# Optimization experiments

Hardware: AMD Instinct MI355X
Metric: run time of the kernel (lower is better)

Reference implementation:

```python
import jax, jax.numpy as jnp
import numpy as np

B, L, C, H = 16, 1024, 512, 8
D = C // H
SCALE = D ** -0.5


def setup_inputs() -> dict:
    key = jax.random.key(0)
    ks = jax.random.split(key, 16)
    s = 0.02  # weight init scale
    inp = {
        "query": jax.random.normal(ks[0], (B, L, C), jnp.float32),
        "query_pos": jax.random.normal(ks[1], (B, L, C), jnp.float32),
        "Wqc": jax.random.normal(ks[2], (C, C), jnp.float32) * s,
        "bqc": jax.random.normal(ks[3], (C,), jnp.float32) * s,
        "Wqp": jax.random.normal(ks[4], (C, C), jnp.float32) * s,
        "bqp": jax.random.normal(ks[5], (C,), jnp.float32) * s,
        "Wkc": jax.random.normal(ks[6], (C, C), jnp.float32) * s,
        "bkc": jax.random.normal(ks[7], (C,), jnp.float32) * s,
        "Wkp": jax.random.normal(ks[8], (C, C), jnp.float32) * s,
        "bkp": jax.random.normal(ks[9], (C,), jnp.float32) * s,
        "Wv": jax.random.normal(ks[10], (C, C), jnp.float32) * s,
        "bv": jax.random.normal(ks[11], (C,), jnp.float32) * s,
        "Wo": jax.random.normal(ks[12], (C, C), jnp.float32) * s,
        "bo": jax.random.normal(ks[13], (C,), jnp.float32) * s,
    }
    return inp


def reference(query, query_pos, Wqc, bqc, Wqp, bqp, Wkc, bkc, Wkp, bkp, Wv, bv, Wo, bo):
    # key = query, value = key, identity = query, key_pos = query_pos (shapes match)
    qc = query @ Wqc.T + bqc          # [B, L, C]
    qp = query_pos @ Wqp.T + bqp
    kc = query @ Wkc.T + bkc
    kp = query_pos @ Wkp.T + bkp
    v = query @ Wv.T + bv

    def split_heads(x):  # [B, L, C] -> [B, H, L, D]
        return x.reshape(B, L, H, D).transpose(0, 2, 1, 3)

    q = split_heads(qc + qp) * SCALE
    k = split_heads(kc + kp)
    vh = split_heads(v)

    attn = jnp.einsum("bhqd,bhkd->bhqk", q, k)
    attn = jax.nn.softmax(attn, axis=-1)
    out = jnp.einsum("bhqk,bhkd->bhqd", attn, vh)  # [B, H, L, D]
    out = out.transpose(0, 2, 1, 3).reshape(B, L, C)
    out = out @ Wo.T + bo
    return query + out
```

## Files before the change

### kernel.cpp

```cpp
#include <hip/hip_runtime.h>

typedef __attribute__((ext_vector_type(8))) short short8;
typedef __attribute__((ext_vector_type(4))) short short4v;
typedef __attribute__((ext_vector_type(4))) float f32x4;
typedef unsigned short u16;

#define QSCALE 0.18033688011112042f

#define BB 16
#define LL 1024
#define CC 512
#define HH 8
#define DD 64
#define MROWS (BB*LL)
#define KPROJ 1024
#define NPROJ 1536

#define WS_XCAT   0ull
#define WS_WCAT   (WS_XCAT + (size_t)MROWS*KPROJ*2)
#define WS_WO     (WS_WCAT + (size_t)NPROJ*KPROJ*2)
#define WS_BIAS   (WS_WO   + (size_t)CC*CC*2)
#define WS_QH     (WS_BIAS + 8192)
#define WS_KH     (WS_QH + (size_t)MROWS*CC*2)
#define WS_VH     (WS_KH + (size_t)MROWS*CC*2)
#define WS_OH     (WS_VH + (size_t)MROWS*CC*2)
#define WS_END    (WS_OH + (size_t)MROWS*CC*2)
#define WS_VT     WS_XCAT

__device__ inline short f2bf(float f) {
  unsigned u = __builtin_bit_cast(unsigned, f);
  u = (u + 0x7FFFu + ((u >> 16) & 1u)) >> 16;
  return (short)u;
}

__device__ inline short8 pack8(const float* src) {
  float4 a = ((const float4*)src)[0];
  float4 b = ((const float4*)src)[1];
  short8 v;
  v[0]=f2bf(a.x); v[1]=f2bf(a.y); v[2]=f2bf(a.z); v[3]=f2bf(a.w);
  v[4]=f2bf(b.x); v[5]=f2bf(b.y); v[6]=f2bf(b.z); v[7]=f2bf(b.w);
  return v;
}

__device__ inline void gload_lds16(const u16* g, char* lds_byte) {
  __builtin_amdgcn_global_load_lds(
      (const __attribute__((address_space(1))) unsigned int*)g,
      (__attribute__((address_space(3))) unsigned int*)lds_byte,
      16, 0, 0);
}


__global__ __launch_bounds__(256) void pack_x_kernel(
    const float* __restrict__ q, const float* __restrict__ qp, u16* __restrict__ xcat) {
  int o = blockIdx.x * 256 + threadIdx.x;
  int row = o >> 7;
  int kk  = (o & 127) << 3;
  const float* src = (kk < 512) ? (q + (size_t)row * 512 + kk)
                                : (qp + (size_t)row * 512 + (kk - 512));
  short8 v = pack8(src);
  *(short8*)(xcat + (size_t)row * KPROJ + kk) = v;
}

__global__ __launch_bounds__(256) void pack_w_kernel(
    const float* __restrict__ Wqc, const float* __restrict__ Wqp,
    const float* __restrict__ Wkc, const float* __restrict__ Wkp,
    const float* __restrict__ Wv,  const float* __restrict__ Wo,
    const float* __restrict__ bqc, const float* __restrict__ bqp,
    const float* __restrict__ bkc, const float* __restrict__ bkp,
    const float* __restrict__ bv,
    u16* __restrict__ wcat, u16* __restrict__ wo_bf, float* __restrict__ bias_cat) {
  int o = blockIdx.x * 256 + threadIdx.x;
  if (o < 196608) {
    int j = o >> 7;
    int kk = (o & 127) << 3;
    const float* src = nullptr;
    if (j < 512)        src = (kk < 512) ? Wqc + (size_t)j * 512 + kk : Wqp + (size_t)j * 512 + (kk - 512);
    else if (j < 1024) { int jj = j - 512;  src = (kk < 512) ? Wkc + (size_t)jj * 512 + kk : Wkp + (size_t)jj * 512 + (kk - 512); }
    else               { int jj = j - 1024; src = (kk < 512) ? Wv  + (size_t)jj * 512 + kk : nullptr; }
    short8 v = {0,0,0,0,0,0,0,0};
    if (src) v = pack8(src);
    *(short8*)(wcat + (size_t)j * KPROJ + kk) = v;
  } else if (o < 229376) {
    int o2 = o - 196608;
    int j = o2 >> 6;
    int kk = (o2 & 63) << 3;
    short8 v = pack8(Wo + (size_t)j * 512 + kk);
    *(short8*)(wo_bf + (size_t)j * 512 + kk) = v;
  }
  if (o < 1536) {
    float v;
    if (o < 512)       v = bqc[o] + bqp[o];
    else if (o < 1024) v = bkc[o - 512] + bkp[o - 512];
    else               v = bv[o - 1024];
    bias_cat[o] = v;
  }
}

template <int KDIM>
__device__ inline void gemm128_loop(const u16* __restrict__ A, const u16* __restrict__ Bw,
                                    int m0, int n0, u16* lds, f32x4 (&acc)[4][4]) {
  const int tid = threadIdx.x;
  const int lane = tid & 63, wave = tid >> 6;
  const int wr = wave >> 1, wc = wave & 1;
  const int lr = lane & 15, lg = lane >> 4;

  auto stage = [&](int buf, int t) {
    int k0 = t * 64;
    #pragma unroll
    for (int i = 0; i < 4; ++i) {
      int s = i * 256 + tid;
      int row = s >> 3, col = s & 7;
      int colp = col ^ (row & 7);
      gload_lds16(A + (size_t)(m0 + row) * KDIM + k0 + colp * 8,
                  (char*)lds + (size_t)buf * 32768 + (size_t)(i * 256 + wave * 64) * 16);
      gload_lds16(Bw + (size_t)(n0 + row) * KDIM + k0 + colp * 8,
                  (char*)lds + (size_t)buf * 32768 + 16384 + (size_t)(i * 256 + wave * 64) * 16);
    }
  };

  auto rdA = [&](int buf, int mf, int ks) {
    int rowl = wr * 64 + mf * 16 + lr;
    int ch = (ks * 4 + lg) ^ (rowl & 7);
    return *(const short8*)(lds + (size_t)buf * 16384 + (size_t)rowl * 64 + ch * 8);
  };
  auto rdB = [&](int buf, int nf, int ks) {
    int rowl = wc * 64 + nf * 16 + lr;
    int ch = (ks * 4 + lg) ^ (rowl & 7);
    return *(const short8*)(lds + (size_t)buf * 16384 + 8192 + (size_t)rowl * 64 + ch * 8);
  };

  stage(0, 0);
  asm volatile("s_waitcnt vmcnt(0)" ::: "memory");
  __builtin_amdgcn_s_barrier();

  constexpr int NT = KDIM / 64;
  int cur = 0;
  for (int t = 0; t < NT; ++t) {
    if (t + 1 < NT) stage(cur ^ 1, t + 1);
    short8 bf[4][2], af[4][2];
    #pragma unroll
    for (int nf = 0; nf < 4; ++nf)
      #pragma unroll
      for (int ks = 0; ks < 2; ++ks) bf[nf][ks] = rdB(cur, nf, ks);
    #pragma unroll
    for (int mf = 0; mf < 4; ++mf)
      #pragma unroll
      for (int ks = 0; ks < 2; ++ks) af[mf][ks] = rdA(cur, mf, ks);
    __builtin_amdgcn_s_setprio(1);
    #pragma unroll
    for (int mf = 0; mf < 4; ++mf)
      #pragma unroll
      for (int nf = 0; nf < 4; ++nf)
        #pragma unroll
        for (int ks = 0; ks < 2; ++ks)
          acc[mf][nf] = __builtin_amdgcn_mfma_f32_16x16x32_bf16(
              bf[nf][ks], af[mf][ks], acc[mf][nf], 0, 0, 0);
    __builtin_amdgcn_s_setprio(0);
    asm volatile("s_waitcnt vmcnt(0)" ::: "memory");
    __builtin_amdgcn_s_barrier();
    cur ^= 1;
  }
}

__global__ __launch_bounds__(256, 2) void proj_gemm_kernel(
    const u16* __restrict__ Xcat, const u16* __restrict__ Wcat,
    const float* __restrict__ bias_cat,
    u16* __restrict__ Qh, u16* __restrict__ Kh, u16* __restrict__ Vh) {
  __shared__ __align__(16) u16 lds[2 * 16384];

  int id0 = blockIdx.x;
  int swz = (id0 & 7) * 192 + (id0 >> 3);
  int bx = swz / 12, by = swz % 12;
  const int m0 = bx * 128, n0 = by * 128;

  const int lane = threadIdx.x & 63, wave = threadIdx.x >> 6;
  const int wr = wave >> 1, wc = wave & 1;
  const int lr = lane & 15, lg = lane >> 4;

  f32x4 acc[4][4];
  f32x4 z4 = {0.f, 0.f, 0.f, 0.f};
  #pragma unroll
  for (int mf = 0; mf < 4; ++mf)
    #pragma unroll
    for (int nf = 0; nf < 4; ++nf) acc[mf][nf] = z4;

  gemm128_loop<KPROJ>(Xcat, Wcat, m0, n0, lds, acc);

  const int cbase = n0 + wc * 64 + lg * 4;
  #pragma unroll
  for (int mf = 0; mf < 4; ++mf) {
    int lglob = m0 + wr * 64 + mf * 16 + lr;
    int bidx = lglob >> 10, lrow = lglob & 1023;
    #pragma unroll
    for (int nf = 0; nf < 4; ++nf) {
      int c = cbase + nf * 16;
      float4 bb = *(const float4*)&bias_cat[c];
      int sec = c >> 9, cj = c & 511;
      int h = cj >> 6, d0 = cj & 63;
      size_t idx = ((size_t)(bidx * HH + h) * LL + lrow) * DD + d0;
      float v0 = acc[mf][nf][0] + bb.x;
      float v1 = acc[mf][nf][1] + bb.y;
      float v2 = acc[mf][nf][2] + bb.z;
      float v3 = acc[mf][nf][3] + bb.w;
      if (sec == 0) { v0 *= QSCALE; v1 *= QSCALE; v2 *= QSCALE; v3 *= QSCALE; }
      short4v o;
      o[0] = f2bf(v0); o[1] = f2bf(v1); o[2] = f2bf(v2); o[3] = f2bf(v3);
      u16* dst = (sec == 0) ? Qh : (sec == 1) ? Kh : Vh;
      *(short4v*)&dst[idx] = o;
    }
  }
}

__global__ __launch_bounds__(256, 2) void out_gemm_kernel(
    const u16* __restrict__ Oh, const u16* __restrict__ Wo_bf,
    const float* __restrict__ bo, const float* __restrict__ query,
    float* __restrict__ out) {
  __shared__ __align__(16) u16 lds[2 * 16384];

  int id0 = blockIdx.x;
  int swz = (id0 & 7) * 64 + (id0 >> 3);
  int bx = swz / 4, by = swz % 4;
  const int m0 = bx * 128, n0 = by * 128;

  const int lane = threadIdx.x & 63, wave = threadIdx.x >> 6;
  const int wr = wave >> 1, wc = wave & 1;
  const int lr = lane & 15, lg = lane >> 4;

  f32x4 acc[4][4];
  f32x4 z4 = {0.f, 0.f, 0.f, 0.f};
  #pragma unroll
  for (int mf = 0; mf < 4; ++mf)
    #pragma unroll
    for (int nf = 0; nf < 4; ++nf) acc[mf][nf] = z4;

  gemm128_loop<CC>(Oh, Wo_bf, m0, n0, lds, acc);

  const int cbase = n0 + wc * 64 + lg * 4;
  #pragma unroll
  for (int mf = 0; mf < 4; ++mf) {
    int rw = m0 + wr * 64 + mf * 16 + lr;
    #pragma unroll
    for (int nf = 0; nf < 4; ++nf) {
      int c = cbase + nf * 16;
      float4 bb = *(const float4*)&bo[c];
      size_t idx = (size_t)rw * CC + c;
      float4 qq = *(const float4*)&query[idx];
      float4 o;
      o.x = acc[mf][nf][0] + bb.x + qq.x;
      o.y = acc[mf][nf][1] + bb.y + qq.y;
      o.z = acc[mf][nf][2] + bb.z + qq.z;
      o.w = acc[mf][nf][3] + bb.w + qq.w;
      *(float4*)&out[idx] = o;
    }
  }
}

__global__ __launch_bounds__(256) void vtrans_kernel(
    const u16* __restrict__ Vh, u16* __restrict__ Vt) {
  __shared__ u16 T[64][72];
  int bh = blockIdx.y;
  int l0 = blockIdx.x * 64;
  int t = threadIdx.x;
  const u16* src = Vh + (size_t)bh * LL * DD;
  {
    int l = t >> 2, dq = (t & 3) * 16;
    short8 v0 = *(const short8*)(src + (size_t)(l0 + l) * DD + dq);
    short8 v1 = *(const short8*)(src + (size_t)(l0 + l) * DD + dq + 8);
    #pragma unroll
    for (int j = 0; j < 8; ++j) T[dq + j][l] = (u16)v0[j];
    #pragma unroll
    for (int j = 0; j < 8; ++j) T[dq + 8 + j][l] = (u16)v1[j];
  }
  __syncthreads();
  {
    int d = t >> 2, lq = (t & 3) * 16;
    u16* dst = Vt + (size_t)bh * DD * LL + (size_t)d * LL + l0 + lq;
    *(short8*)dst = *(const short8*)&T[d][lq];
    *(short8*)(dst + 8) = *(const short8*)&T[d][lq + 8];
  }
}

__global__ __launch_bounds__(256, 2) void attn_kernel(
    const u16* __restrict__ Qh, const u16* __restrict__ Kh,
    const u16* __restrict__ Vt, u16* __restrict__ Oh) {
  __shared__ __align__(16) u16 Kl[2][64 * 64];
  __shared__ __align__(16) u16 Vl[2][64 * 64];
  __shared__ __align__(16) char Pp[4][8192];

  const int tid = threadIdx.x;
  const int lane = tid & 63, wave = tid >> 6;
  const int lr = lane & 15, lg = lane >> 4;
  const int sw = (lr & 7) * 2;
  int n = blockIdx.x;
  int rest = n >> 3;
  const int bh = (n & 7) * 16 + (rest >> 2);
  const int q0 = (rest & 3) * 256;

  const u16* Qb = Qh + (size_t)bh * LL * DD;
  const u16* Kb = Kh + (size_t)bh * LL * DD;
  const u16* Vb = Vt + (size_t)bh * DD * LL;

  short8 aq[4][2];
  #pragma unroll
  for (int m = 0; m < 4; ++m)
    #pragma unroll
    for (int s = 0; s < 2; ++s)
      aq[m][s] = *(const short8*)(Qb + (size_t)(q0 + wave * 64 + m * 16 + lr) * DD + s * 32 + lg * 8);

  f32x4 z4 = {0.f, 0.f, 0.f, 0.f};
  f32x4 oaccT[4][4];
  #pragma unroll
  for (int m = 0; m < 4; ++m)
    #pragma unroll
    for (int db = 0; db < 4; ++db) oaccT[m][db] = z4;
  float lsums[4] = {0.f, 0.f, 0.f, 0.f};

  auto stage = [&](int buf, int kt) {
    int kk0 = kt * 64;
    #pragma unroll
    for (int i = 0; i < 2; ++i) {
      int c = i * 256 + wave * 64 + lane;
      int row = c >> 3, koct = c & 7;
      int ks = koct ^ (row & 7);
      gload_lds16(Kb + (size_t)(kk0 + row) * DD + ks * 8,
                  (char*)&Kl[buf][0] + (size_t)(i * 4 + wave) * 1024);
      gload_lds16(Vb + (size_t)row * LL + kk0 + ks * 8,
                  (char*)&Vl[buf][0] + (size_t)(i * 4 + wave) * 1024);
    }
  };

  stage(0, 0);
  int cur = 0;
  char* Pw = &Pp[wave][0];
  for (int kt = 0; kt < 16; ++kt) {
    if (kt + 1 < 16) {
      stage(cur ^ 1, kt + 1);
      asm volatile("s_waitcnt vmcnt(4)" ::: "memory");
    } else {
      asm volatile("s_waitcnt vmcnt(0)" ::: "memory");
    }
    __builtin_amdgcn_s_barrier();
    __builtin_amdgcn_sched_barrier(0);

    short8 ka[2][4];
    #pragma unroll
    for (int s = 0; s < 2; ++s)
      #pragma unroll
      for (int kb = 0; kb < 4; ++kb) {
        int key = kb * 16 + lr;
        int dct = s * 4 + lg;
        ka[s][kb] = *(const short8*)((const char*)&Kl[cur][0] + (size_t)key * 128 + ((dct ^ (key & 7)) << 4));
      }
    f32x4 ps[4][4];
    #pragma unroll
    for (int m = 0; m < 4; ++m)
      #pragma unroll
      for (int kb = 0; kb < 4; ++kb) ps[m][kb] = z4;
    __builtin_amdgcn_s_setprio(1);
    #pragma unroll
    for (int s = 0; s < 2; ++s)
      #pragma unroll
      for (int kb = 0; kb < 4; ++kb)
        #pragma unroll
        for (int m = 0; m < 4; ++m)
          ps[m][kb] = __builtin_amdgcn_mfma_f32_16x16x32_bf16(ka[s][kb], aq[m][s], ps[m][kb], 0, 0, 0);
    __builtin_amdgcn_s_setprio(0);

    #pragma unroll
    for (int m = 0; m < 4; ++m) {
      #pragma unroll
      for (int kb = 0; kb < 4; ++kb) {
        float p0, p1, p2, p3;
        asm("v_exp_f32 %0, %1" : "=v"(p0) : "v"(ps[m][kb][0]));
        asm("v_exp_f32 %0, %1" : "=v"(p1) : "v"(ps[m][kb][1]));
        asm("v_exp_f32 %0, %1" : "=v"(p2) : "v"(ps[m][kb][2]));
        asm("v_exp_f32 %0, %1" : "=v"(p3) : "v"(ps[m][kb][3]));
        lsums[m] += (p0 + p1) + (p2 + p3);
        unsigned lo, hi;
        asm("v_cvt_pk_bf16_f32 %0, %1, %2" : "=v"(lo) : "v"(p0), "v"(p1));
        asm("v_cvt_pk_bf16_f32 %0, %1, %2" : "=v"(hi) : "v"(p2), "v"(p3));
        uint2 w; w.x = lo; w.y = hi;
        *(uint2*)(Pw + m * 2048 + lr * 128 + ((((kb * 4 + lg) ^ sw)) << 3)) = w;
      }
    }

    short8 bv[2][4];
    #pragma unroll
    for (int s = 0; s < 2; ++s)
      #pragma unroll
      for (int db = 0; db < 4; ++db) {
        int d = db * 16 + lr;
        int kct = s * 4 + lg;
        bv[s][db] = *(const short8*)((const char*)&Vl[cur][0] + (size_t)d * 128 + ((kct ^ (d & 7)) << 4));
      }

    asm volatile("s_waitcnt lgkmcnt(0)" ::: "memory");
    __builtin_amdgcn_sched_barrier(0);

    __builtin_amdgcn_s_setprio(1);
    #pragma unroll
    for (int m = 0; m < 4; ++m) {
      #pragma unroll
      for (int s = 0; s < 2; ++s) {
        int val0 = s * 8 + lg * 2;
        uint4 pw = *(const uint4*)(Pw + m * 2048 + lr * 128 + (((val0 ^ sw)) << 3));
        short8 ap = __builtin_bit_cast(short8, pw);
        #pragma unroll
        for (int db = 0; db < 4; ++db)
          oaccT[m][db] = __builtin_amdgcn_mfma_f32_16x16x32_bf16(bv[s][db], ap, oaccT[m][db], 0, 0, 0);
      }
    }
    __builtin_amdgcn_s_setprio(0);

    __builtin_amdgcn_s_barrier();
    cur ^= 1;
  }

  int b = bh >> 3, h = bh & 7;
  #pragma unroll
  for (int m = 0; m < 4; ++m) {
    float v = lsums[m];
    v += __shfl_xor(v, 16);
    v += __shfl_xor(v, 32);
    float inv = 1.0f / v;
    int q = q0 + wave * 64 + m * 16 + lr;
    #pragma unroll
    for (int db = 0; db < 4; ++db) {
      int d0 = db * 16 + lg * 4;
      short4v o;
      #pragma unroll
      for (int r = 0; r < 4; ++r) o[r] = f2bf(oaccT[m][db][r] * inv);
      *(short4v*)&Oh[(size_t)(b * LL + q) * CC + h * 64 + d0] = o;
    }
  }
}

extern "C" void kernel_launch(void* const* d_in, const int* in_sizes, int n_in,
                              void* d_out, int out_size, void* d_ws, size_t ws_size,
                              hipStream_t stream) {
  (void)in_sizes; (void)n_in; (void)out_size;
  const float* query = (const float*)d_in[0];
  const float* qpos  = (const float*)d_in[1];
  const float* Wqc = (const float*)d_in[2];
  const float* bqc = (const float*)d_in[3];
  const float* Wqp = (const float*)d_in[4];
  const float* bqp = (const float*)d_in[5];
  const float* Wkc = (const float*)d_in[6];
  const float* bkc = (const float*)d_in[7];
  const float* Wkp = (const float*)d_in[8];
  const float* bkp = (const float*)d_in[9];
  const float* Wv  = (const float*)d_in[10];
  const float* bv  = (const float*)d_in[11];
  const float* Wo  = (const float*)d_in[12];
  const float* bo  = (const float*)d_in[13];

  char* ws = (char*)d_ws;
  if (ws_size < WS_END) return;

  u16*   Xcat     = (u16*)(ws + WS_XCAT);
  u16*   Wcat     = (u16*)(ws + WS_WCAT);
  u16*   Wo_bf    = (u16*)(ws + WS_WO);
  float* bias_cat = (float*)(ws + WS_BIAS);
  u16*   Qh       = (u16*)(ws + WS_QH);
  u16*   Kh       = (u16*)(ws + WS_KH);
  u16*   Vh       = (u16*)(ws + WS_VH);
  u16*   Oh       = (u16*)(ws + WS_OH);
  u16*   Vtr      = (u16*)(ws + WS_VT);
  float* out      = (float*)d_out;

  pack_x_kernel<<<dim3(8192), dim3(256), 0, stream>>>(query, qpos, Xcat);
  pack_w_kernel<<<dim3(896), dim3(256), 0, stream>>>(Wqc, Wqp, Wkc, Wkp, Wv, Wo,
                                                     bqc, bqp, bkc, bkp, bv,
                                                     Wcat, Wo_bf, bias_cat);
  proj_gemm_kernel<<<dim3((MROWS / 128) * (NPROJ / 128)), dim3(256), 0, stream>>>(
      Xcat, Wcat, bias_cat, Qh, Kh, Vh);
  vtrans_kernel<<<dim3(LL / 64, BB * HH), dim3(256), 0, stream>>>(Vh, Vtr);
  attn_kernel<<<dim3(512), dim3(256), 0, stream>>>(Qh, Kh, Vtr, Oh);
  out_gemm_kernel<<<dim3((MROWS / 128) * (CC / 128)), dim3(256), 0, stream>>>(
      Oh, Wo_bf, bo, query, out);
}
```

Measured before the change: 159.4 us.

## Fuse V transpose into projection GEMM epilogue and merge pack kernels

The projection GEMM epilogue for V-column tiles now transposes the tile through LDS and writes V directly in the [b,h,d,l] layout the attention kernel consumes. This removes the separate vtrans kernel and the round trip of V through global memory. The two packing kernels are merged into one launch to save a kernel launch. The cost is extra LDS traffic and a barrier in the epilogue of the V blocks, which creates divergent work between block types.

```diff
diff --git a/kernel.cpp b/kernel.cpp
--- a/kernel.cpp
+++ b/kernel.cpp
@@ -22,10 +22,9 @@
 #define WS_BIAS   (WS_WO   + (size_t)CC*CC*2)
 #define WS_QH     (WS_BIAS + 8192)
 #define WS_KH     (WS_QH + (size_t)MROWS*CC*2)
-#define WS_VH     (WS_KH + (size_t)MROWS*CC*2)
-#define WS_OH     (WS_VH + (size_t)MROWS*CC*2)
+#define WS_VT     (WS_KH + (size_t)MROWS*CC*2)
+#define WS_OH     (WS_VT + (size_t)MROWS*CC*2)
 #define WS_END    (WS_OH + (size_t)MROWS*CC*2)
-#define WS_VT     WS_XCAT
 
 __device__ inline short f2bf(float f) {
   unsigned u = __builtin_bit_cast(unsigned, f);
@@ -49,27 +48,27 @@
       16, 0, 0);
 }
 
-
-__global__ __launch_bounds__(256) void pack_x_kernel(
-    const float* __restrict__ q, const float* __restrict__ qp, u16* __restrict__ xcat) {
-  int o = blockIdx.x * 256 + threadIdx.x;
-  int row = o >> 7;
-  int kk  = (o & 127) << 3;
-  const float* src = (kk < 512) ? (q + (size_t)row * 512 + kk)
-                                : (qp + (size_t)row * 512 + (kk - 512));
-  short8 v = pack8(src);
-  *(short8*)(xcat + (size_t)row * KPROJ + kk) = v;
-}
-
-__global__ __launch_bounds__(256) void pack_w_kernel(
+__global__ __launch_bounds__(256) void pack_all_kernel(
+    const float* __restrict__ q, const float* __restrict__ qp,
     const float* __restrict__ Wqc, const float* __restrict__ Wqp,
     const float* __restrict__ Wkc, const float* __restrict__ Wkp,
     const float* __restrict__ Wv,  const float* __restrict__ Wo,
     const float* __restrict__ bqc, const float* __restrict__ bqp,
     const float* __restrict__ bkc, const float* __restrict__ bkp,
     const float* __restrict__ bv,
-    u16* __restrict__ wcat, u16* __restrict__ wo_bf, float* __restrict__ bias_cat) {
-  int o = blockIdx.x * 256 + threadIdx.x;
+    u16* __restrict__ xcat, u16* __restrict__ wcat, u16* __restrict__ wo_bf,
+    float* __restrict__ bias_cat) {
+  if (blockIdx.x < 8192) {
+    int o = blockIdx.x * 256 + threadIdx.x;
+    int row = o >> 7;
+    int kk  = (o & 127) << 3;
+    const float* src = (kk < 512) ? (q + (size_t)row * 512 + kk)
+                                  : (qp + (size_t)row * 512 + (kk - 512));
+    short8 v = pack8(src);
+    *(short8*)(xcat + (size_t)row * KPROJ + kk) = v;
+    return;
+  }
+  int o = (blockIdx.x - 8192) * 256 + threadIdx.x;
   if (o < 196608) {
     int j = o >> 7;
     int kk = (o & 127) << 3;
@@ -165,7 +164,7 @@
 __global__ __launch_bounds__(256, 2) void proj_gemm_kernel(
     const u16* __restrict__ Xcat, const u16* __restrict__ Wcat,
     const float* __restrict__ bias_cat,
-    u16* __restrict__ Qh, u16* __restrict__ Kh, u16* __restrict__ Vh) {
+    u16* __restrict__ Qh, u16* __restrict__ Kh, u16* __restrict__ Vt) {
   __shared__ __align__(16) u16 lds[2 * 16384];
 
   int id0 = blockIdx.x;
@@ -173,7 +172,8 @@
   int bx = swz / 12, by = swz % 12;
   const int m0 = bx * 128, n0 = by * 128;
 
-  const int lane = threadIdx.x & 63, wave = threadIdx.x >> 6;
+  const int tid = threadIdx.x;
+  const int lane = tid & 63, wave = tid >> 6;
   const int wr = wave >> 1, wc = wave & 1;
   const int lr = lane & 15, lg = lane >> 4;
 
@@ -186,27 +186,57 @@
 
   gemm128_loop<KPROJ>(Xcat, Wcat, m0, n0, lds, acc);
 
-  const int cbase = n0 + wc * 64 + lg * 4;
-  #pragma unroll
-  for (int mf = 0; mf < 4; ++mf) {
-    int lglob = m0 + wr * 64 + mf * 16 + lr;
-    int bidx = lglob >> 10, lrow = lglob & 1023;
-    #pragma unroll
-    for (int nf = 0; nf < 4; ++nf) {
-      int c = cbase + nf * 16;
-      float4 bb = *(const float4*)&bias_cat[c];
-      int sec = c >> 9, cj = c & 511;
-      int h = cj >> 6, d0 = cj & 63;
-      size_t idx = ((size_t)(bidx * HH + h) * LL + lrow) * DD + d0;
-      float v0 = acc[mf][nf][0] + bb.x;
-      float v1 = acc[mf][nf][1] + bb.y;
-      float v2 = acc[mf][nf][2] + bb.z;
-      float v3 = acc[mf][nf][3] + bb.w;
-      if (sec == 0) { v0 *= QSCALE; v1 *= QSCALE; v2 *= QSCALE; v3 *= QSCALE; }
-      short4v o;
-      o[0] = f2bf(v0); o[1] = f2bf(v1); o[2] = f2bf(v2); o[3] = f2bf(v3);
-      u16* dst = (sec == 0) ? Qh : (sec == 1) ? Kh : Vh;
-      *(short4v*)&dst[idx] = o;
+  if (n0 < 1024) {
+    const int cbase = n0 + wc * 64 + lg * 4;
+    #pragma unroll
+    for (int mf = 0; mf < 4; ++mf) {
+      int lglob = m0 + wr * 64 + mf * 16 + lr;
+      int bidx = lglob >> 10, lrow = lglob & 1023;
+      #pragma unroll
+      for (int nf = 0; nf < 4; ++nf) {
+        int c = cbase + nf * 16;
+        float4 bb = *(const float4*)&bias_cat[c];
+        int sec = c >> 9, cj = c & 511;
+        int h = cj >> 6, d0 = cj & 63;
+        size_t idx = ((size_t)(bidx * HH + h) * LL + lrow) * DD + d0;
+        float v0 = acc[mf][nf][0] + bb.x;
+        float v1 = acc[mf][nf][1] + bb.y;
+        float v2 = acc[mf][nf][2] + bb.z;
+        float v3 = acc[mf][nf][3] + bb.w;
+        if (sec == 0) { v0 *= QSCALE; v1 *= QSCALE; v2 *= QSCALE; v3 *= QSCALE; }
+        short4v o;
+        o[0] = f2bf(v0); o[1] = f2bf(v1); o[2] = f2bf(v2); o[3] = f2bf(v3);
+        u16* dst = (sec == 0) ? Qh : Kh;
+        *(short4v*)&dst[idx] = o;
+      }
+    }
+  } else {
+    u16* T = lds;
+    #pragma unroll
+    for (int mf = 0; mf < 4; ++mf) {
+      int ll = wr * 64 + mf * 16 + lr;
+      #pragma unroll
+      for (int nf = 0; nf < 4; ++nf) {
+        int cjl = wc * 64 + nf * 16 + lg * 4;
+        int c = n0 + cjl;
+        float4 bb = *(const float4*)&bias_cat[c];
+        T[(size_t)(cjl + 0) * 136 + ll] = (u16)f2bf(acc[mf][nf][0] + bb.x);
+        T[(size_t)(cjl + 1) * 136 + ll] = (u16)f2bf(acc[mf][nf][1] + bb.y);
+        T[(size_t)(cjl + 2) * 136 + ll] = (u16)f2bf(acc[mf][nf][2] + bb.z);
+        T[(size_t)(cjl + 3) * 136 + ll] = (u16)f2bf(acc[mf][nf][3] + bb.w);
+      }
+    }
+    __builtin_amdgcn_s_barrier();
+    int b = m0 >> 10, lrow0 = m0 & 1023;
+    #pragma unroll
+    for (int i = 0; i < 8; ++i) {
+      int c2 = i * 256 + tid;
+      int r = c2 >> 4;
+      int o8 = (c2 & 15) * 8;
+      short8 v = *(const short8*)&T[(size_t)r * 136 + o8];
+      int cj = n0 - 1024 + r;
+      int h = cj >> 6, d = cj & 63;
+      *(short8*)&Vt[((size_t)(b * HH + h) * DD + d) * LL + lrow0 + o8] = v;
     }
   }
 }
@@ -252,31 +282,6 @@
       o.w = acc[mf][nf][3] + bb.w + qq.w;
       *(float4*)&out[idx] = o;
     }
-  }
-}
-
-__global__ __launch_bounds__(256) void vtrans_kernel(
-    const u16* __restrict__ Vh, u16* __restrict__ Vt) {
-  __shared__ u16 T[64][72];
-  int bh = blockIdx.y;
-  int l0 = blockIdx.x * 64;
-  int t = threadIdx.x;
-  const u16* src = Vh + (size_t)bh * LL * DD;
-  {
-    int l = t >> 2, dq = (t & 3) * 16;
-    short8 v0 = *(const short8*)(src + (size_t)(l0 + l) * DD + dq);
-    short8 v1 = *(const short8*)(src + (size_t)(l0 + l) * DD + dq + 8);
-    #pragma unroll
-    for (int j = 0; j < 8; ++j) T[dq + j][l] = (u16)v0[j];
-    #pragma unroll
-    for (int j = 0; j < 8; ++j) T[dq + 8 + j][l] = (u16)v1[j];
-  }
-  __syncthreads();
-  {
-    int d = t >> 2, lq = (t & 3) * 16;
-    u16* dst = Vt + (size_t)bh * DD * LL + (size_t)d * LL + l0 + lq;
-    *(short8*)dst = *(const short8*)&T[d][lq];
-    *(short8*)(dst + 8) = *(const short8*)&T[d][lq + 8];
   }
 }
 
@@ -463,18 +468,15 @@
   float* bias_cat = (float*)(ws + WS_BIAS);
   u16*   Qh       = (u16*)(ws + WS_QH);
   u16*   Kh       = (u16*)(ws + WS_KH);
-  u16*   Vh       = (u16*)(ws + WS_VH);
+  u16*   Vtr      = (u16*)(ws + WS_VT);
   u16*   Oh       = (u16*)(ws + WS_OH);
-  u16*   Vtr      = (u16*)(ws + WS_VT);
   float* out      = (float*)d_out;
 
-  pack_x_kernel<<<dim3(8192), dim3(256), 0, stream>>>(query, qpos, Xcat);
-  pack_w_kernel<<<dim3(896), dim3(256), 0, stream>>>(Wqc, Wqp, Wkc, Wkp, Wv, Wo,
-                                                     bqc, bqp, bkc, bkp, bv,
-                                                     Wcat, Wo_bf, bias_cat);
+  pack_all_kernel<<<dim3(9088), dim3(256), 0, stream>>>(
+      query, qpos, Wqc, Wqp, Wkc, Wkp, Wv, Wo,
+      bqc, bqp, bkc, bkp, bv, Xcat, Wcat, Wo_bf, bias_cat);
   proj_gemm_kernel<<<dim3((MROWS / 128) * (NPROJ / 128)), dim3(256), 0, stream>>>(
-      Xcat, Wcat, bias_cat, Qh, Kh, Vh);
-  vtrans_kernel<<<dim3(LL / 64, BB * HH), dim3(256), 0, stream>>>(Vh, Vtr);
+      Xcat, Wcat, bias_cat, Qh, Kh, Vtr);
   attn_kernel<<<dim3(512), dim3(256), 0, stream>>>(Qh, Kh, Vtr, Oh);
   out_gemm_kernel<<<dim3((MROWS / 128) * (CC / 128)), dim3(256), 0, stream>>>(
       Oh, Wo_bf, bo, query, out);
```

Measured after the change: 150.7 us. -5.5%, faster.
